# Kernel tuning notes

Hardware: AMD Instinct MI355X
Metric: run time of the kernel (lower is better)

The kernel has to match this reference:

```python
import jax, jax.numpy as jnp
import numpy as np

EPS = 1e-8
ANGULAR_WEIGHT = 0.1
L2_REG = 1e-4


def gram_schmidt_batch(A):
    # A: (B, 3, 3); orthogonalize the COLUMNS
    u1 = A[:, :, 0]
    e1 = u1 / (jnp.linalg.norm(u1, axis=1, keepdims=True) + EPS)
    a2 = A[:, :, 1]
    u2 = a2 - jnp.sum(e1 * a2, axis=1, keepdims=True) * e1
    e2 = u2 / (jnp.linalg.norm(u2, axis=1, keepdims=True) + EPS)
    a3 = A[:, :, 2]
    u3 = a3 - jnp.sum(e1 * a3, axis=1, keepdims=True) * e1 - jnp.sum(e2 * a3, axis=1, keepdims=True) * e2
    e3 = u3 / (jnp.linalg.norm(u3, axis=1, keepdims=True) + EPS)
    Q = jnp.stack([e1, e2, e3], axis=2)  # (B,3,3), columns e1,e2,e3
    det = jnp.linalg.det(Q)
    # flip third column where det < 0 to ensure proper rotation
    e3_fixed = jnp.where(det[:, None] < 0, -Q[:, :, 2], Q[:, :, 2])
    return Q.at[:, :, 2].set(e3_fixed)


def nine_d_to_rotmat(nine_d):
    A = jnp.clip(nine_d, -10.0, 10.0).reshape(-1, 3, 3)
    return gram_schmidt_batch(A)


def angular_distance(pred_9d, target_9d):
    pred_rot = nine_d_to_rotmat(pred_9d)
    target_rot = nine_d_to_rotmat(target_9d)
    # trace(pred^T @ target) = sum over all entries of elementwise product
    traces = jnp.einsum('bij,bij->b', pred_rot, target_rot)
    traces = jnp.clip(traces, -3.0 + 1e-6, 3.0 - 1e-6)
    cos_angle = jnp.clip((traces - 1.0) / 2.0, -1.0 + 1e-7, 1.0 - 1e-7)
    angles_deg = jnp.arccos(cos_angle) * (180.0 / np.pi)
    return jnp.where(jnp.isnan(angles_deg), 180.0, angles_deg)


def orthogonality_loss(nine_d):
    B = nine_d.shape[0]
    M = nine_d.reshape(B, 3, 3)
    AtA = jnp.einsum('bki,bkj->bij', M, M)
    diff = AtA - jnp.eye(3, dtype=nine_d.dtype)
    return jnp.mean(jnp.sum(diff * diff, axis=(1, 2)))


def setup_inputs() -> dict:
    key = jax.random.key(0)
    k1, k2 = jax.random.split(key)
    B = 4194304
    return {
        'pred_delta_9d': jax.random.normal(k1, (B, 9), dtype=jnp.float32),
        'target_delta_9d': jax.random.normal(k2, (B, 9), dtype=jnp.float32),
    }


def reference(pred_delta_9d, target_delta_9d):
    pred_delta_9d = jnp.clip(pred_delta_9d, -10.0, 10.0)
    pred_rot = nine_d_to_rotmat(pred_delta_9d)
    target_rot = nine_d_to_rotmat(target_delta_9d)
    diff = pred_rot - target_rot
    chordal_loss = jnp.mean(jnp.sum(diff * diff, axis=(1, 2)))
    angular_loss_term = jnp.mean(angular_distance(pred_delta_9d, target_delta_9d))
    ortho_loss = orthogonality_loss(pred_delta_9d)
    l2_loss = jnp.mean(pred_delta_9d ** 2)
    total_loss = chordal_loss + ANGULAR_WEIGHT * angular_loss_term + 0.01 * ortho_loss + L2_REG * l2_loss
    # NaN fallback: MSE between pred and target
    fallback = jnp.mean((pred_delta_9d - target_delta_9d) ** 2)
    return jnp.where(jnp.isnan(total_loss), fallback, total_loss)
```

## Files before the change

kernel.cpp:

```cpp
#include <hip/hip_runtime.h>
#include <math.h>

#define EPS_GS 1e-8f
#define RAD2DEG 57.29577951308232f
#define PI_F 3.14159265358979f

constexpr int THREADS   = 256;
constexpr int TILE_ROTS = 256;
constexpr int TILE_F    = TILE_ROTS * 9;
constexpr int TILE_TOT  = TILE_F * 2;
constexpr int CHUNK_F   = 256;
constexpr int CHUNKS    = TILE_TOT / CHUNK_F;
constexpr int NSLOTS    = 16;
constexpr int MAX_BLKS  = 1024;

__device__ __forceinline__ float clip10(float x) {
    x = x < -10.f ? -10.f : x;
    x = x >  10.f ?  10.f : x;
    return x;
}

__device__ __forceinline__ float fsqrt(float x) { return __builtin_amdgcn_sqrtf(x); }
__device__ __forceinline__ float frcp(float x)  { return __builtin_amdgcn_rcpf(x); }

__device__ __forceinline__ void gload_lds16(const float* g, float* l) {
    __builtin_amdgcn_global_load_lds(
        (const __attribute__((address_space(1))) void*)g,
        (__attribute__((address_space(3))) void*)l,
        16, 0, 0);
}

__device__ __forceinline__ float fast_acos(float x) {
    float ax = fabsf(x);
    float p = fmaf(ax, -0.0187293f, 0.0742610f);
    p = fmaf(ax, p, -0.2121144f);
    p = fmaf(ax, p, 1.5707288f);
    float pos = fsqrt(1.f - ax) * p;
    return x >= 0.f ? pos : PI_F - pos;
}

__device__ __forceinline__ void gs_rotmat(const float* v, float* R) {
    float c0x = v[0], c0y = v[3], c0z = v[6];
    float c1x = v[1], c1y = v[4], c1z = v[7];
    float c2x = v[2], c2y = v[5], c2z = v[8];

    float s1 = fmaf(c0x, c0x, fmaf(c0y, c0y, c0z*c0z));
    float inv1 = frcp(fsqrt(s1) + EPS_GS);
    float e1x = c0x*inv1, e1y = c0y*inv1, e1z = c0z*inv1;

    float d = fmaf(e1x, c1x, fmaf(e1y, c1y, e1z*c1z));
    float u2x = fmaf(-d, e1x, c1x), u2y = fmaf(-d, e1y, c1y), u2z = fmaf(-d, e1z, c1z);
    float s2 = fmaf(u2x, u2x, fmaf(u2y, u2y, u2z*u2z));
    float inv2 = frcp(fsqrt(s2) + EPS_GS);
    float e2x = u2x*inv2, e2y = u2y*inv2, e2z = u2z*inv2;

    float d1 = fmaf(e1x, c2x, fmaf(e1y, c2y, e1z*c2z));
    float d2 = fmaf(e2x, c2x, fmaf(e2y, c2y, e2z*c2z));
    float u3x = fmaf(-d1, e1x, fmaf(-d2, e2x, c2x));
    float u3y = fmaf(-d1, e1y, fmaf(-d2, e2y, c2y));
    float u3z = fmaf(-d1, e1z, fmaf(-d2, e2z, c2z));
    float s3 = fmaf(u3x, u3x, fmaf(u3y, u3y, u3z*u3z));
    float inv3 = frcp(fsqrt(s3) + EPS_GS);
    float e3x = u3x*inv3, e3y = u3y*inv3, e3z = u3z*inv3;

    float cxx = e2y*e3z - e2z*e3y;
    float cxy = e2z*e3x - e2x*e3z;
    float cxz = e2x*e3y - e2y*e3x;
    float det = fmaf(e1x, cxx, fmaf(e1y, cxy, e1z*cxz));
    if (det < 0.f) { e3x = -e3x; e3y = -e3y; e3z = -e3z; }

    R[0] = e1x; R[1] = e2x; R[2] = e3x;
    R[3] = e1y; R[4] = e2y; R[5] = e3y;
    R[6] = e1z; R[7] = e2z; R[8] = e3z;
}

__device__ __forceinline__ void accum_rot(const float* pr, const float* tg,
                                          float& lt, float& lf) {
    float pc[9], tc[9];
    #pragma unroll
    for (int m = 0; m < 9; ++m) { pc[m] = clip10(pr[m]); tc[m] = clip10(tg[m]); }

    float Rp[9], Rt[9];
    gs_rotmat(pc, Rp);
    gs_rotmat(tc, Rt);

    float chord = 0.f, tr = 0.f;
    #pragma unroll
    for (int m = 0; m < 9; ++m) {
        float d = Rp[m] - Rt[m];
        chord = fmaf(d, d, chord);
        tr    = fmaf(Rp[m], Rt[m], tr);
    }

    const float trLo = -3.0f + 1e-6f, trHi = 3.0f - 1e-6f;
    tr = tr < trLo ? trLo : (tr > trHi ? trHi : tr);
    float ca = (tr - 1.f) * 0.5f;
    const float cLo = -1.0f + 1e-7f, cHi = 1.0f - 1e-7f;
    ca = ca < cLo ? cLo : (ca > cHi ? cHi : ca);
    float ang = fast_acos(ca) * RAD2DEG;
    if (ang != ang) ang = 180.f;

    float o = 0.f;
    #pragma unroll
    for (int i = 0; i < 3; ++i) {
        float dii = fmaf(pc[i], pc[i], fmaf(pc[3+i], pc[3+i], pc[6+i]*pc[6+i])) - 1.f;
        o = fmaf(dii, dii, o);
    }
    #pragma unroll
    for (int i = 0; i < 3; ++i) {
        #pragma unroll
        for (int j = i + 1; j < 3; ++j) {
            float s = fmaf(pc[i], pc[j], fmaf(pc[3+i], pc[3+j], pc[6+i]*pc[6+j]));
            float s2 = s + s;
            o = fmaf(s2, s, o);
        }
    }

    float l2 = 0.f, fb = 0.f;
    #pragma unroll
    for (int m = 0; m < 9; ++m) {
        l2 = fmaf(pc[m], pc[m], l2);
        float d = pc[m] - tg[m];
        fb = fmaf(d, d, fb);
    }

    lt += fmaf(0.1f, ang, chord) + fmaf(0.01f, o, (1e-4f/9.f)*l2);
    lf += fb;
}

__global__ __launch_bounds__(THREADS, 4)
void rot_loss_kernel(const float* __restrict__ pred, const float* __restrict__ targ,
                     double* __restrict__ acc, int B) {
    __shared__ float buf[2][TILE_TOT];
    __shared__ float rsum_t[4], rsum_f[4];

    const int tid    = threadIdx.x;
    const int wv     = tid >> 6;
    const int lane   = tid & 63;
    const int ntiles = (B + TILE_ROTS - 1) / TILE_ROTS;
    const int tstep  = gridDim.x;

    float lt = 0.f, lf = 0.f;

    auto tile_full = [&](int t) {
        return (size_t)(t + 1) * TILE_ROTS <= (size_t)B;
    };
    auto stage = [&](int b, int t) {
        const float* psrc = pred + (size_t)t * TILE_F;
        const float* qsrc = targ + (size_t)t * TILE_F;
        if (wv < 2) {
            #pragma unroll
            for (int k = 0; k < 5; ++k) {
                const int c = wv*5 + k;
                const float* src = (c < 9) ? (psrc + (size_t)c * CHUNK_F)
                                           : (qsrc + (size_t)(c - 9) * CHUNK_F);
                gload_lds16(src + lane*4, &buf[b][c * CHUNK_F]);
            }
        } else {
            #pragma unroll
            for (int k = 0; k < 4; ++k) {
                const int c = 10 + (wv-2)*4 + k;
                const float* src = (c < 9) ? (psrc + (size_t)c * CHUNK_F)
                                           : (qsrc + (size_t)(c - 9) * CHUNK_F);
                gload_lds16(src + lane*4, &buf[b][c * CHUNK_F]);
            }
        }
    };

    const int t0 = blockIdx.x;
    int cur = 0;
    if (t0 < ntiles && tile_full(t0)) stage(0, t0);

    for (int t = t0; t < ntiles; t += tstep) {
        if (tile_full(t)) {
            const int tn = t + tstep;
            const bool nx = (tn < ntiles) && tile_full(tn);
            if (nx) {
                stage(cur ^ 1, tn);
                if (wv < 2) asm volatile("s_waitcnt vmcnt(5)" ::: "memory");
                else        asm volatile("s_waitcnt vmcnt(4)" ::: "memory");
            } else {
                asm volatile("s_waitcnt vmcnt(0)" ::: "memory");
            }
            __builtin_amdgcn_s_barrier();
            asm volatile("" ::: "memory");
            accum_rot(&buf[cur][9*tid], &buf[cur][TILE_F + 9*tid], lt, lf);
            asm volatile("" ::: "memory");
            __builtin_amdgcn_s_barrier();
            cur ^= 1;
        } else {
            const size_t rot0 = (size_t)t * TILE_ROTS;
            const int rem = (int)((size_t)B - rot0);
            for (int r = tid; r < rem; r += THREADS) {
                float a1[9], b1[9];
                const float* pp = pred + (rot0 + r) * 9;
                const float* qq = targ + (rot0 + r) * 9;
                for (int m = 0; m < 9; ++m) { a1[m] = pp[m]; b1[m] = qq[m]; }
                accum_rot(a1, b1, lt, lf);
            }
        }
    }

    #pragma unroll
    for (int off = 32; off > 0; off >>= 1) {
        lt += __shfl_down(lt, off, 64);
        lf += __shfl_down(lf, off, 64);
    }
    if (lane == 0) { rsum_t[wv] = lt; rsum_f[wv] = lf; }
    __syncthreads();
    if (tid == 0) {
        float bt = rsum_t[0] + rsum_t[1] + rsum_t[2] + rsum_t[3];
        float bf = rsum_f[0] + rsum_f[1] + rsum_f[2] + rsum_f[3];
        double* slot = acc + (size_t)(blockIdx.x & (NSLOTS - 1)) * 8;
        unsafeAtomicAdd(&slot[0], (double)bt);
        unsafeAtomicAdd(&slot[1], (double)bf);
    }
}

__global__ void finalize_kernel(const double* __restrict__ acc,
                                float* __restrict__ out, int B) {
    if (threadIdx.x == 0 && blockIdx.x == 0) {
        double t = 0.0, f = 0.0;
        for (int s = 0; s < NSLOTS; ++s) { t += acc[s*8]; f += acc[s*8 + 1]; }
        double total = t / (double)B;
        double fb    = f / (9.0 * (double)B);
        out[0] = isnan(total) ? (float)fb : (float)total;
    }
}

extern "C" void kernel_launch(void* const* d_in, const int* in_sizes, int n_in,
                              void* d_out, int out_size, void* d_ws, size_t ws_size,
                              hipStream_t stream) {
    const float* pred = (const float*)d_in[0];
    const float* targ = (const float*)d_in[1];
    const int n = in_sizes[0];
    const int B = n / 9;

    double* acc = (double*)d_ws;
    hipMemsetAsync(d_ws, 0, NSLOTS * 8 * sizeof(double), stream);

    const int ntiles = (B + TILE_ROTS - 1) / TILE_ROTS;
    const int blocks = ntiles < MAX_BLKS ? ntiles : MAX_BLKS;
    rot_loss_kernel<<<blocks, THREADS, 0, stream>>>(pred, targ, acc, B);
    finalize_kernel<<<1, 64, 0, stream>>>(acc, (float*)d_out, B);
}
```

Baseline: 312.2 us.

## Make LDS staging wave-private and drop block barriers

Each wave now stages only its own 64 rotations (pred and target) into a private LDS region, using two 16-byte and one 4-byte global_load_lds per input. Because no wave reads another wave's data, the two block-wide s_barriers per tile are removed. Each wave waits on vmcnt(0), copies its rows from LDS into registers, then issues the prefetch for the next tile before computing. This is meant to remove barrier stalls and let waves drift independently, at the cost of a full vmcnt wait that leaves the prefetch overlapping only the compute of the current tile.

```diff
diff --git a/kernel.cpp b/kernel.cpp
--- a/kernel.cpp
+++ b/kernel.cpp
@@ -8,9 +8,7 @@
 constexpr int THREADS   = 256;
 constexpr int TILE_ROTS = 256;
 constexpr int TILE_F    = TILE_ROTS * 9;
-constexpr int TILE_TOT  = TILE_F * 2;
-constexpr int CHUNK_F   = 256;
-constexpr int CHUNKS    = TILE_TOT / CHUNK_F;
+constexpr int WAVE_F    = 64 * 9;
 constexpr int NSLOTS    = 16;
 constexpr int MAX_BLKS  = 1024;
 
@@ -28,6 +26,12 @@
         (const __attribute__((address_space(1))) void*)g,
         (__attribute__((address_space(3))) void*)l,
         16, 0, 0);
+}
+__device__ __forceinline__ void gload_lds4(const float* g, float* l) {
+    __builtin_amdgcn_global_load_lds(
+        (const __attribute__((address_space(1))) void*)g,
+        (__attribute__((address_space(3))) void*)l,
+        4, 0, 0);
 }
 
 __device__ __forceinline__ float fast_acos(float x) {
@@ -131,7 +135,7 @@
 __global__ __launch_bounds__(THREADS, 4)
 void rot_loss_kernel(const float* __restrict__ pred, const float* __restrict__ targ,
                      double* __restrict__ acc, int B) {
-    __shared__ float buf[2][TILE_TOT];
+    __shared__ alignas(16) float buf[2][4][2][WAVE_F];
     __shared__ float rsum_t[4], rsum_f[4];
 
     const int tid    = threadIdx.x;
@@ -146,25 +150,16 @@
         return (size_t)(t + 1) * TILE_ROTS <= (size_t)B;
     };
     auto stage = [&](int b, int t) {
-        const float* psrc = pred + (size_t)t * TILE_F;
-        const float* qsrc = targ + (size_t)t * TILE_F;
-        if (wv < 2) {
-            #pragma unroll
-            for (int k = 0; k < 5; ++k) {
-                const int c = wv*5 + k;
-                const float* src = (c < 9) ? (psrc + (size_t)c * CHUNK_F)
-                                           : (qsrc + (size_t)(c - 9) * CHUNK_F);
-                gload_lds16(src + lane*4, &buf[b][c * CHUNK_F]);
-            }
-        } else {
-            #pragma unroll
-            for (int k = 0; k < 4; ++k) {
-                const int c = 10 + (wv-2)*4 + k;
-                const float* src = (c < 9) ? (psrc + (size_t)c * CHUNK_F)
-                                           : (qsrc + (size_t)(c - 9) * CHUNK_F);
-                gload_lds16(src + lane*4, &buf[b][c * CHUNK_F]);
-            }
-        }
+        const float* ps = pred + (size_t)t * TILE_F + (size_t)wv * WAVE_F;
+        const float* qs = targ + (size_t)t * TILE_F + (size_t)wv * WAVE_F;
+        float* dp = &buf[b][wv][0][0];
+        float* dq = &buf[b][wv][1][0];
+        gload_lds16(ps +       lane*4, dp);
+        gload_lds16(ps + 256 + lane*4, dp + 256);
+        gload_lds4 (ps + 512 + lane,   dp + 512);
+        gload_lds16(qs +       lane*4, dq);
+        gload_lds16(qs + 256 + lane*4, dq + 256);
+        gload_lds4 (qs + 512 + lane,   dq + 512);
     };
 
     const int t0 = blockIdx.x;
@@ -173,20 +168,16 @@
 
     for (int t = t0; t < ntiles; t += tstep) {
         if (tile_full(t)) {
+            asm volatile("s_waitcnt vmcnt(0)" ::: "memory");
+            float a1[9], b1[9];
+            #pragma unroll
+            for (int m = 0; m < 9; ++m) a1[m] = buf[cur][wv][0][lane*9 + m];
+            #pragma unroll
+            for (int m = 0; m < 9; ++m) b1[m] = buf[cur][wv][1][lane*9 + m];
+            asm volatile("" ::: "memory");
             const int tn = t + tstep;
-            const bool nx = (tn < ntiles) && tile_full(tn);
-            if (nx) {
-                stage(cur ^ 1, tn);
-                if (wv < 2) asm volatile("s_waitcnt vmcnt(5)" ::: "memory");
-                else        asm volatile("s_waitcnt vmcnt(4)" ::: "memory");
-            } else {
-                asm volatile("s_waitcnt vmcnt(0)" ::: "memory");
-            }
-            __builtin_amdgcn_s_barrier();
-            asm volatile("" ::: "memory");
-            accum_rot(&buf[cur][9*tid], &buf[cur][TILE_F + 9*tid], lt, lf);
-            asm volatile("" ::: "memory");
-            __builtin_amdgcn_s_barrier();
+            if (tn < ntiles && tile_full(tn)) stage(cur ^ 1, tn);
+            accum_rot(a1, b1, lt, lf);
             cur ^= 1;
         } else {
             const size_t rot0 = (size_t)t * TILE_ROTS;
```

After: 313.0 us. About the same (+0.3%).
